# Performance work log

Measured on AMD Instinct MI355X. Metric: run time of the kernel, lower is better.

## Reference

```python
import jax, jax.numpy as jnp
import numpy as np

D_MODEL = 1024
D_STATE = 16
EXPAND = 2
D_INNER = D_MODEL * EXPAND
DT_RANK = D_MODEL // 16


def setup_inputs() -> dict:
    key = jax.random.key(0)
    ks = jax.random.split(key, 12)
    B, T = 2, 2048
    s_in = 1.0 / np.sqrt(D_MODEL)
    s_x = 1.0 / np.sqrt(D_INNER)
    s_dt = 1.0 / np.sqrt(DT_RANK)
    inp = {
        'u': jax.random.normal(ks[0], (B, T, D_MODEL), jnp.float32),
        'W_in': jax.random.uniform(ks[1], (2 * D_INNER, D_MODEL), jnp.float32, -s_in, s_in),
        'b_in': jax.random.uniform(ks[2], (2 * D_INNER,), jnp.float32, -s_in, s_in),
        'W_x': jax.random.uniform(ks[3], (DT_RANK + 2 * D_STATE, D_INNER), jnp.float32, -s_x, s_x),
        'b_x': jax.random.uniform(ks[4], (DT_RANK + 2 * D_STATE,), jnp.float32, -s_x, s_x),
        'W_dt': jax.random.uniform(ks[5], (D_INNER, DT_RANK), jnp.float32, -s_dt, s_dt),
        'b_dt': jax.random.uniform(ks[6], (D_INNER,), jnp.float32, -s_dt, s_dt),
        'A_log': jnp.log(jnp.abs(jax.random.normal(ks[7], (D_INNER, D_STATE), jnp.float32)) + 1e-6),
        'D': jnp.ones((D_INNER,), jnp.float32),
        'W_out': jax.random.uniform(ks[8], (D_MODEL, D_INNER), jnp.float32, -s_x, s_x),
        'b_out': jax.random.uniform(ks[9], (D_MODEL,), jnp.float32, -s_x, s_x),
    }
    return inp


def _ssm_forward(u, W_in, b_in, W_x, b_x, W_dt, b_dt, A_log, D, W_out, b_out):
    B, T, _ = u.shape
    u_inner = u @ W_in.T + b_in                       # [B,T,2*d_inner]
    x, z = jnp.split(u_inner, 2, axis=-1)             # each [B,T,d_inner]
    dbc = x @ W_x.T + b_x                             # [B,T,dt_rank+2N]
    delta_raw = dbc[..., :DT_RANK]
    B_ssm = dbc[..., DT_RANK:DT_RANK + D_STATE]       # [B,T,N]
    C_ssm = dbc[..., DT_RANK + D_STATE:]              # [B,T,N]
    delta = jax.nn.softplus(delta_raw @ W_dt.T + b_dt)  # [B,T,d_inner]
    A = -jnp.exp(A_log)                               # [d_inner,N]

    def step(h, xs):
        dt_t, x_t, Bt, Ct = xs                        # [B,d], [B,d], [B,N], [B,N]
        dA = jnp.exp(dt_t[..., None] * A)             # [B,d,N]
        dB = dt_t[..., None] * Bt[:, None, :]         # [B,d,N]
        h = h * dA + x_t[..., None] * dB
        y_t = jnp.einsum('bdn,bn->bd', h, Ct)
        return h, y_t

    h0 = jnp.zeros((B, D_INNER, D_STATE), u.dtype)
    xs = (jnp.swapaxes(delta, 0, 1), jnp.swapaxes(x, 0, 1),
          jnp.swapaxes(B_ssm, 0, 1), jnp.swapaxes(C_ssm, 0, 1))
    _, y = jax.lax.scan(step, h0, xs)                 # y: [T,B,d_inner]
    y = jnp.swapaxes(y, 0, 1)                         # [B,T,d_inner]
    y = y + x * D
    y = y * (z * jax.nn.sigmoid(z))                   # SiLU gate
    return y @ W_out.T + b_out                        # [B,T,d_model]


def reference(u, W_in, b_in, W_x, b_x, W_dt, b_dt, A_log, D, W_out, b_out):
    return _ssm_forward(u, W_in, b_in, W_x, b_x, W_dt, b_dt, A_log, D, W_out, b_out)
```

## Files before the change

kernel.cpp:

```cpp
#include <hip/hip_runtime.h>
#include <math.h>

#define BATCH 2
#define SEQ   2048
#define DM    1024
#define DI    2048
#define NST   16
#define MT    (BATCH*SEQ)
#define CHK   64
#define LCH   (SEQ/CHK)

typedef __attribute__((ext_vector_type(8))) short  bf16x8;
typedef __attribute__((ext_vector_type(4))) float  f32x4;

static __device__ __forceinline__ unsigned short f2bf(float f) {
  unsigned u = __float_as_uint(f);
  u += 0x7fff + ((u >> 16) & 1);
  return (unsigned short)(u >> 16);
}
static __device__ __forceinline__ float bf2f(unsigned short h) {
  return __uint_as_float(((unsigned)h) << 16);
}
static __device__ __forceinline__ float fexp2(float x) {
  float r;
  asm("v_exp_f32 %0, %1" : "=v"(r) : "v"(x));
  return r;
}
static __device__ __forceinline__ float flog2(float x) {
  float r;
  asm("v_log_f32 %0, %1" : "=v"(r) : "v"(x));
  return r;
}

#define SEG_U    (MT*DM/4)
#define SEG_WIN  (2*DI*DM/4)
#define SEG_WOUT (DM*DI/4)
#define SEG_WX   (96*DI/4)
#define SEG_WDT  (DI*64/4)
#define SEG_A    (DI*NST/4)
#define CUM0 SEG_U
#define CUM1 (CUM0+SEG_WIN)
#define CUM2 (CUM1+SEG_WOUT)
#define CUM3 (CUM2+SEG_WX)
#define CUM4 (CUM3+SEG_WDT)
#define CUM5 (CUM4+SEG_A)

__global__ __launch_bounds__(256) void convall_kernel(
    const float* __restrict__ u, const float* __restrict__ W_in,
    const float* __restrict__ W_out, const float* __restrict__ W_x,
    const float* __restrict__ W_dt, const float* __restrict__ A_log,
    unsigned short* __restrict__ u_bf, unsigned short* __restrict__ win_bf,
    unsigned short* __restrict__ wout_bf, unsigned short* __restrict__ wx_bf,
    unsigned short* __restrict__ wdt_bf, float* __restrict__ A2tab)
{
  const int gid = blockIdx.x*256 + threadIdx.x;
  const float4* src; ushort4* dst; int idx;
  if (gid < CUM0)      { idx = gid;        src = (const float4*)u;     dst = (ushort4*)u_bf; }
  else if (gid < CUM1) { idx = gid - CUM0; src = (const float4*)W_in;  dst = (ushort4*)win_bf; }
  else if (gid < CUM2) { idx = gid - CUM1; src = (const float4*)W_out; dst = (ushort4*)wout_bf; }
  else if (gid < CUM3) { idx = gid - CUM2; src = (const float4*)W_x;   dst = (ushort4*)wx_bf; }
  else if (gid < CUM4) { idx = gid - CUM3; src = (const float4*)W_dt;  dst = (ushort4*)wdt_bf; }
  else if (gid < CUM5) {
    int i = gid - CUM4;
    float4 v = ((const float4*)A_log)[i];
    float4 o;
    o.x = -1.44269504f * __expf(v.x);
    o.y = -1.44269504f * __expf(v.y);
    o.z = -1.44269504f * __expf(v.z);
    o.w = -1.44269504f * __expf(v.w);
    ((float4*)A2tab)[i] = o;
    return;
  } else return;
  float4 v = src[idx];
  ushort4 o;
  o.x = f2bf(v.x); o.y = f2bf(v.y); o.z = f2bf(v.z); o.w = f2bf(v.w);
  dst[idx] = o;
}

#define MEMFENCE asm volatile("" ::: "memory")

template<int K>
__global__ __launch_bounds__(512, 2) void gemm3_kernel(
    const unsigned short* __restrict__ A,
    const unsigned short* __restrict__ B,
    const float* __restrict__ bias,
    unsigned short* __restrict__ Cout, int nbx)
{
  extern __shared__ unsigned short smem[];
  unsigned short* As = smem;
  unsigned short* Bs = smem + 4*256*32;
  constexpr int NT = K / 32;

  const int nwg = gridDim.x;
  const int cpx = nwg >> 3;
  const int bid = blockIdx.x;
  const int swz = (bid & 7) * cpx + (bid >> 3);
  const int bx = swz % nbx;
  const int by = swz / nbx;

  const int tid  = threadIdx.x;
  const int lane = tid & 63;
  const int wid  = tid >> 6;
  const int wr   = wid >> 2;
  const int wc   = wid & 3;

  const size_t arow0 = (size_t)by * 256;
  const size_t brow0 = (size_t)bx * 256;

  const int s_r4 = lane >> 2;
  const int s_c  = lane & 3;

  auto STAGE_A = [&](int slot, int T) {
#pragma unroll
    for (int i = 0; i < 2; ++i) {
      const int r  = wid*32 + i*16 + s_r4;
      const int lc = s_c ^ ((r >> 1) & 3);
      const unsigned short* g = A + (arow0 + r)*(size_t)K + T*32 + lc*8;
      __builtin_amdgcn_global_load_lds(
          (const __attribute__((address_space(1))) void*)g,
          (__attribute__((address_space(3))) void*)(As + slot*(256*32) + (wid*32 + i*16)*32),
          16, 0, 0);
    }
  };
  auto STAGE_B = [&](int slot, int T) {
#pragma unroll
    for (int i = 0; i < 2; ++i) {
      const int r  = wid*32 + i*16 + s_r4;
      const int lc = s_c ^ ((r >> 1) & 3);
      const unsigned short* g = B + (brow0 + r)*(size_t)K + T*32 + lc*8;
      __builtin_amdgcn_global_load_lds(
          (const __attribute__((address_space(1))) void*)g,
          (__attribute__((address_space(3))) void*)(Bs + slot*(256*32) + (wid*32 + i*16)*32),
          16, 0, 0);
    }
  };

  f32x4 zero = {0.f, 0.f, 0.f, 0.f};
  f32x4 acc[8][4];
#pragma unroll
  for (int i = 0; i < 8; ++i)
#pragma unroll
    for (int j = 0; j < 4; ++j) acc[i][j] = zero;

  STAGE_A(0, 0); STAGE_B(0, 0);
  STAGE_A(1, 1); STAGE_B(1, 1);
  STAGE_A(2, 2); STAGE_B(2, 2);
  asm volatile("s_waitcnt vmcnt(8)" ::: "memory");
  __builtin_amdgcn_s_barrier();
  MEMFENCE;

  const int lrow = lane & 15, k8 = lane >> 4;
  bf16x8 bfr[4];

  for (int t = 0; t < NT; ++t) {
    const int slot = t & 3;
    const int sts  = (t + 3) & 3;
    const unsigned short* Asl = As + slot*(256*32);
    const unsigned short* Bsl = Bs + slot*(256*32);

    bf16x8 af[4];
#pragma unroll
    for (int nj = 0; nj < 4; ++nj) {
      const int r = wc*64 + nj*16 + lrow;
      bfr[nj] = *(const bf16x8*)&Bsl[r*32 + (k8 ^ ((r >> 1) & 3))*8];
    }
#pragma unroll
    for (int mi = 0; mi < 4; ++mi) {
      const int r = wr*128 + mi*16 + lrow;
      af[mi] = *(const bf16x8*)&Asl[r*32 + (k8 ^ ((r >> 1) & 3))*8];
    }
    if (t + 3 < NT) STAGE_A(sts, t + 3);
    MEMFENCE;
    __builtin_amdgcn_s_setprio(1);
#pragma unroll
    for (int mi = 0; mi < 4; ++mi)
#pragma unroll
      for (int nj = 0; nj < 4; ++nj)
        acc[mi][nj] = __builtin_amdgcn_mfma_f32_16x16x32_bf16(
                          af[mi], bfr[nj], acc[mi][nj], 0, 0, 0);
    __builtin_amdgcn_s_setprio(0);
    MEMFENCE;

#pragma unroll
    for (int mi = 0; mi < 4; ++mi) {
      const int r = wr*128 + 64 + mi*16 + lrow;
      af[mi] = *(const bf16x8*)&Asl[r*32 + (k8 ^ ((r >> 1) & 3))*8];
    }
    if (t + 3 < NT) STAGE_B(sts, t + 3);
    MEMFENCE;
    __builtin_amdgcn_s_setprio(1);
#pragma unroll
    for (int mi = 0; mi < 4; ++mi)
#pragma unroll
      for (int nj = 0; nj < 4; ++nj)
        acc[mi + 4][nj] = __builtin_amdgcn_mfma_f32_16x16x32_bf16(
                              af[mi], bfr[nj], acc[mi + 4][nj], 0, 0, 0);
    __builtin_amdgcn_s_setprio(0);

    if (t <= NT - 4)      asm volatile("s_waitcnt vmcnt(8)" ::: "memory");
    else if (t == NT - 3) asm volatile("s_waitcnt vmcnt(4)" ::: "memory");
    else                  asm volatile("s_waitcnt vmcnt(0)" ::: "memory");
    __builtin_amdgcn_s_barrier();
    MEMFENCE;
  }

  const int lcol = lane & 15, lrq = lane >> 4;
#pragma unroll
  for (int nj = 0; nj < 4; ++nj) {
    const int colg = bx*256 + wc*64 + nj*16 + lcol;
    const float bv = bias[colg];
#pragma unroll
    for (int mi = 0; mi < 8; ++mi) {
      const int rowg = by*256 + wr*128 + mi*16 + lrq*4;
#pragma unroll
      for (int q = 0; q < 4; ++q)
        Cout[(size_t)(rowg + q)*4096 + colg] = f2bf(acc[mi][nj][q] + bv);
    }
  }
}

template<int BN, int BK, bool OUT_BF16, int LDC, int ACT>
__global__ __launch_bounds__(256, 4) void gemm2_kernel(
    const unsigned short* __restrict__ A,
    const unsigned short* __restrict__ B,
    const float* __restrict__ bias,
    void* __restrict__ Cout, int K, int nbx)
{
  constexpr int NH = BK / 32;
  constexpr int NJ = BN / 32;
  __shared__ unsigned short Abuf[2][NH][128*32];
  __shared__ unsigned short Bbuf[2][NH][BN*32];

  const int nwg = gridDim.x;
  const int cpx = nwg >> 3;
  const int bid = blockIdx.x;
  const int swz = (bid & 7) * cpx + (bid >> 3);
  const int bx = swz % nbx;
  const int by = swz / nbx;

  const int tid  = threadIdx.x;
  const int lane = tid & 63;
  const int wid  = tid >> 6;
  const int wr   = wid >> 1;
  const int wc   = wid & 1;
  const int lr    = lane >> 2;
  const int lslot = lane & 3;

  f32x4 zero = {0.f, 0.f, 0.f, 0.f};
  f32x4 acc[4][NJ];
#pragma unroll
  for (int i = 0; i < 4; ++i)
#pragma unroll
    for (int j = 0; j < NJ; ++j) acc[i][j] = zero;

  const size_t arow0 = (size_t)by * 128;
  const size_t brow0 = (size_t)bx * BN;
  const int NT = K / BK;

  auto STAGE = [&](int buf, int k0) {
#pragma unroll
    for (int half = 0; half < NH; ++half) {
#pragma unroll
      for (int i = 0; i < 2; ++i) {
        const int Rb = (wid + i*4) * 16;
        const int r  = Rb + lr;
        const int c8 = lslot ^ ((r >> 1) & 3);
        const unsigned short* ga = A + (arow0 + r)*(size_t)K + k0 + half*32 + c8*8;
        __builtin_amdgcn_global_load_lds(
            (const __attribute__((address_space(1))) void*)ga,
            (__attribute__((address_space(3))) void*)(&Abuf[buf][half][Rb*32]),
            16, 0, 0);
      }
#pragma unroll
      for (int i = 0; i < BN/64; ++i) {
        const int Rb = (wid + i*4) * 16;
        const int r  = Rb + lr;
        const int c8 = lslot ^ ((r >> 1) & 3);
        const unsigned short* gb = B + (brow0 + r)*(size_t)K + k0 + half*32 + c8*8;
        __builtin_amdgcn_global_load_lds(
            (const __attribute__((address_space(1))) void*)gb,
            (__attribute__((address_space(3))) void*)(&Bbuf[buf][half][Rb*32]),
            16, 0, 0);
      }
    }
  };

  STAGE(0, 0);
  __syncthreads();

  const int lrow = lane & 15, k8 = lane >> 4;
  int cur = 0;
  for (int kt = 0; kt < NT; ++kt) {
    if (kt + 1 < NT) STAGE(cur ^ 1, (kt + 1) * BK);

#pragma unroll
    for (int half = 0; half < NH; ++half) {
      bf16x8 af[4], bfr[NJ];
#pragma unroll
      for (int mi = 0; mi < 4; ++mi) {
        const int r = wr*64 + mi*16 + lrow;
        af[mi] = *(const bf16x8*)&Abuf[cur][half][r*32 + (k8 ^ ((r >> 1) & 3))*8];
      }
#pragma unroll
      for (int nj = 0; nj < NJ; ++nj) {
        const int r = wc*(BN/2) + nj*16 + lrow;
        bfr[nj] = *(const bf16x8*)&Bbuf[cur][half][r*32 + (k8 ^ ((r >> 1) & 3))*8];
      }
      __builtin_amdgcn_s_setprio(1);
#pragma unroll
      for (int mi = 0; mi < 4; ++mi)
#pragma unroll
        for (int nj = 0; nj < NJ; ++nj)
          acc[mi][nj] = __builtin_amdgcn_mfma_f32_16x16x32_bf16(
                            af[mi], bfr[nj], acc[mi][nj], 0, 0, 0);
      __builtin_amdgcn_s_setprio(0);
    }
    __syncthreads();
    cur ^= 1;
  }

  const int lcol = lane & 15, lrq = lane >> 4;
#pragma unroll
  for (int nj = 0; nj < NJ; ++nj) {
    const int colg = bx*BN + wc*(BN/2) + nj*16 + lcol;
    const float bv = bias[colg];
#pragma unroll
    for (int mi = 0; mi < 4; ++mi) {
      const int rowg = by*128 + wr*64 + mi*16 + lrq*4;
#pragma unroll
      for (int q = 0; q < 4; ++q) {
        float v = acc[mi][nj][q] + bv;
        if constexpr (ACT == 1) {
          float e = fexp2(-1.44269504f * fabsf(v));
          v = fmaxf(v, 0.f) + 0.69314718f * flog2(1.f + e);
        }
        if constexpr (OUT_BF16)
          ((unsigned short*)Cout)[(size_t)(rowg + q)*LDC + colg] = f2bf(v);
        else
          ((float*)Cout)[(size_t)(rowg + q)*LDC + colg] = v;
      }
    }
  }
}

__global__ __launch_bounds__(256) void dbc_mfma_kernel(
    const unsigned short* __restrict__ A,
    const unsigned short* __restrict__ Bw,
    float* __restrict__ partial)
{
  __shared__ unsigned short Abuf[64*32];
  __shared__ unsigned short Bbuf[96*32];

  const int tid  = threadIdx.x;
  const int lane = tid & 63;
  const int wid  = tid >> 6;
  const int lr    = lane >> 2;
  const int lslot = lane & 3;
  const size_t arow0 = (size_t)blockIdx.x * 64;
  const int ks   = blockIdx.y;
  const int k0b  = ks * (DI/4);

  f32x4 zero = {0.f, 0.f, 0.f, 0.f};
  f32x4 acc[6];
#pragma unroll
  for (int j = 0; j < 6; ++j) acc[j] = zero;

  for (int k0 = k0b; k0 < k0b + DI/4; k0 += 32) {
    {
      const int Rb = wid*16;
      const int r  = Rb + lr;
      const int c8 = lslot ^ ((r >> 1) & 3);
      const unsigned short* ga = A + (arow0 + r)*4096 + k0 + c8*8;
      __builtin_amdgcn_global_load_lds(
          (const __attribute__((address_space(1))) void*)ga,
          (__attribute__((address_space(3))) void*)(Abuf + Rb*32), 16, 0, 0);
    }
    if (wid < 3) {
#pragma unroll
      for (int i = 0; i < 2; ++i) {
        const int Rb = wid*32 + i*16;
        const int r  = Rb + lr;
        const int c8 = lslot ^ ((r >> 1) & 3);
        const unsigned short* gb = Bw + (size_t)r*DI + k0 + c8*8;
        __builtin_amdgcn_global_load_lds(
            (const __attribute__((address_space(1))) void*)gb,
            (__attribute__((address_space(3))) void*)(Bbuf + Rb*32), 16, 0, 0);
      }
    }
    __syncthreads();

    const int lrow = lane & 15, k8 = lane >> 4;
    const int ra = wid*16 + lrow;
    bf16x8 af = *(const bf16x8*)&Abuf[ra*32 + (k8 ^ ((ra >> 1) & 3))*8];
#pragma unroll
    for (int nj = 0; nj < 6; ++nj) {
      const int rb = nj*16 + lrow;
      bf16x8 bf_ = *(const bf16x8*)&Bbuf[rb*32 + (k8 ^ ((rb >> 1) & 3))*8];
      acc[nj] = __builtin_amdgcn_mfma_f32_16x16x32_bf16(af, bf_, acc[nj], 0, 0, 0);
    }
    __syncthreads();
  }

  const int lcol = lane & 15, lrq = lane >> 4;
  const int rowg = (int)arow0 + wid*16 + lrq*4;
#pragma unroll
  for (int nj = 0; nj < 6; ++nj) {
    const int colg = nj*16 + lcol;
#pragma unroll
    for (int q = 0; q < 4; ++q)
      partial[((size_t)ks*MT + rowg + q)*96 + colg] = acc[nj][q];
  }
}

__global__ __launch_bounds__(256) void dbc_reduce_kernel(
    const float* __restrict__ partial, const float* __restrict__ bx,
    float* __restrict__ dbc, unsigned short* __restrict__ draw_bf)
{
  const int gid = blockIdx.x*256 + threadIdx.x;
  const int m = gid / 96;
  const int c = gid - m*96;
  const size_t stride = (size_t)MT*96;
  float s = partial[gid] + partial[gid + stride]
          + partial[gid + 2*stride] + partial[gid + 3*stride] + bx[c];
  if (c < 64) draw_bf[(size_t)m*64 + c] = f2bf(s);
  else        dbc[(size_t)m*96 + c] = s;
}

__global__ __launch_bounds__(256) void scanA_kernel(
    const unsigned short* __restrict__ uib,
    const float* __restrict__ dbc,
    const unsigned short* __restrict__ delta_bf,
    const float* __restrict__ A2tab,
    float* __restrict__ P,
    float* __restrict__ S)
{
  __shared__ float Bsh[LCH][16];
  const int bid = blockIdx.x;
  const int d   = (bid & 7)*256 + threadIdx.x;
  const int c   = (bid >> 3) & (CHK-1);
  const int b   = bid >> 9;
  const int t0  = c * LCH;

  {
    int i = threadIdx.x;
    if (i < LCH*4) {
      int st = i >> 2, p = i & 3;
      float4 v = *(const float4*)(dbc + ((size_t)b*SEQ + t0 + st)*96 + 64 + p*4);
      *(float4*)&Bsh[st][p*4] = v;
    }
  }

  float A2[NST];
  {
    const float4* ap = (const float4*)(A2tab + (size_t)d*NST);
#pragma unroll
    for (int q = 0; q < 4; ++q) {
      float4 v = ap[q];
      A2[q*4+0] = v.x; A2[q*4+1] = v.y; A2[q*4+2] = v.z; A2[q*4+3] = v.w;
    }
  }

  float h[NST];
#pragma unroll
  for (int nn = 0; nn < NST; ++nn) h[nn] = 0.f;
  float sdt = 0.f;

  const unsigned short* dptr = delta_bf + ((size_t)b*SEQ + t0)*DI + d;
  const unsigned short* xptr = uib      + ((size_t)b*SEQ + t0)*4096 + d;

  float dt = bf2f(dptr[0]);
  float xv = bf2f(xptr[0]);
  __syncthreads();

  for (int t = 0; t < LCH; ++t) {
    const float dtc = dt, xvc = xv;
    if (t + 1 < LCH) {
      const size_t tn = (size_t)(t+1);
      dt = bf2f(dptr[tn*DI]);
      xv = bf2f(xptr[tn*4096]);
    }
    float4 Bv0 = *(const float4*)&Bsh[t][0];
    float4 Bv1 = *(const float4*)&Bsh[t][4];
    float4 Bv2 = *(const float4*)&Bsh[t][8];
    float4 Bv3 = *(const float4*)&Bsh[t][12];
    float Bc[NST] = {Bv0.x,Bv0.y,Bv0.z,Bv0.w, Bv1.x,Bv1.y,Bv1.z,Bv1.w,
                     Bv2.x,Bv2.y,Bv2.z,Bv2.w, Bv3.x,Bv3.y,Bv3.z,Bv3.w};
    sdt += dtc;
    const float xdt = xvc * dtc;
#pragma unroll
    for (int nn = 0; nn < NST; ++nn) {
      float dA = fexp2(dtc * A2[nn]);
      h[nn] = h[nn]*dA + xdt*Bc[nn];
    }
  }

  float* Pp = P + (((size_t)b*CHK + c)*DI + d)*NST;
  float* Sp = S + (((size_t)b*CHK + c)*DI + d)*NST;
#pragma unroll
  for (int q = 0; q < 4; ++q) {
    float4 pv = { fexp2(A2[q*4+0]*sdt), fexp2(A2[q*4+1]*sdt),
                  fexp2(A2[q*4+2]*sdt), fexp2(A2[q*4+3]*sdt) };
    float4 sv = { h[q*4+0], h[q*4+1], h[q*4+2], h[q*4+3] };
    *(float4*)(Pp + q*4) = pv;
    *(float4*)(Sp + q*4) = sv;
  }
}

__global__ __launch_bounds__(256) void scanB_kernel(
    const float* __restrict__ P, float* __restrict__ S)
{
  const int gid = blockIdx.x*256 + threadIdx.x;
  const int n4 = gid & 3;
  const int d  = (gid >> 2) & (DI-1);
  const int b  = gid >> 13;

  float4 h = {0.f, 0.f, 0.f, 0.f};
  for (int c = 0; c < CHK; ++c) {
    const size_t idx = (((size_t)b*CHK + c)*DI + d)*NST + n4*4;
    float4 p = *(const float4*)(P + idx);
    float4 s = *(const float4*)(S + idx);
    *(float4*)(S + idx) = h;
    h.x = h.x*p.x + s.x;
    h.y = h.y*p.y + s.y;
    h.z = h.z*p.z + s.z;
    h.w = h.w*p.w + s.w;
  }
}

__global__ __launch_bounds__(256) void scanC_kernel(
    const unsigned short* __restrict__ uib,
    const float* __restrict__ dbc,
    const unsigned short* __restrict__ delta_bf,
    const float* __restrict__ A2tab,
    const float* __restrict__ Dp,
    const float* __restrict__ S,
    unsigned short* __restrict__ y_bf)
{
  __shared__ float BCs[LCH][32];
  const int bid = blockIdx.x;
  const int d   = (bid & 7)*256 + threadIdx.x;
  const int c   = (bid >> 3) & (CHK-1);
  const int b   = bid >> 9;
  const int t0  = c * LCH;

  {
    int i = threadIdx.x;
    int st = i >> 3, p = i & 7;
    float4 v = *(const float4*)(dbc + ((size_t)b*SEQ + t0 + st)*96 + 64 + p*4);
    *(float4*)&BCs[st][p*4] = v;
  }

  float A2[NST];
  {
    const float4* ap = (const float4*)(A2tab + (size_t)d*NST);
#pragma unroll
    for (int q = 0; q < 4; ++q) {
      float4 v = ap[q];
      A2[q*4+0] = v.x; A2[q*4+1] = v.y; A2[q*4+2] = v.z; A2[q*4+3] = v.w;
    }
  }
  const float Dv = Dp[d];

  float h[NST];
  {
    const float* Sp = S + (((size_t)b*CHK + c)*DI + d)*NST;
#pragma unroll
    for (int q = 0; q < 4; ++q) {
      float4 sv = *(const float4*)(Sp + q*4);
      h[q*4+0] = sv.x; h[q*4+1] = sv.y; h[q*4+2] = sv.z; h[q*4+3] = sv.w;
    }
  }

  const unsigned short* dptr = delta_bf + ((size_t)b*SEQ + t0)*DI + d;
  const unsigned short* xptr = uib      + ((size_t)b*SEQ + t0)*4096 + d;
  unsigned short* yp         = y_bf     + ((size_t)b*SEQ + t0)*DI + d;

  float dt = bf2f(dptr[0]);
  float xv = bf2f(xptr[0]);
  float zv = bf2f(xptr[2048]);
  __syncthreads();

  for (int t = 0; t < LCH; ++t) {
    const float dtc = dt, xvc = xv, zvc = zv;
    if (t + 1 < LCH) {
      const size_t tn = (size_t)(t+1);
      dt = bf2f(dptr[tn*DI]);
      xv = bf2f(xptr[tn*4096]);
      zv = bf2f(xptr[tn*4096 + 2048]);
    }
    float4 Bv0 = *(const float4*)&BCs[t][0];
    float4 Bv1 = *(const float4*)&BCs[t][4];
    float4 Bv2 = *(const float4*)&BCs[t][8];
    float4 Bv3 = *(const float4*)&BCs[t][12];
    float4 Cv0 = *(const float4*)&BCs[t][16];
    float4 Cv1 = *(const float4*)&BCs[t][20];
    float4 Cv2 = *(const float4*)&BCs[t][24];
    float4 Cv3 = *(const float4*)&BCs[t][28];
    float Bc[NST] = {Bv0.x,Bv0.y,Bv0.z,Bv0.w, Bv1.x,Bv1.y,Bv1.z,Bv1.w,
                     Bv2.x,Bv2.y,Bv2.z,Bv2.w, Bv3.x,Bv3.y,Bv3.z,Bv3.w};
    float Cc[NST] = {Cv0.x,Cv0.y,Cv0.z,Cv0.w, Cv1.x,Cv1.y,Cv1.z,Cv1.w,
                     Cv2.x,Cv2.y,Cv2.z,Cv2.w, Cv3.x,Cv3.y,Cv3.z,Cv3.w};
    const float xdt = xvc * dtc;
    float y = 0.f;
#pragma unroll
    for (int nn = 0; nn < NST; ++nn) {
      float dA = fexp2(dtc * A2[nn]);
      h[nn] = h[nn]*dA + xdt*Bc[nn];
      y += h[nn]*Cc[nn];
    }
    y += xvc * Dv;
    y *= zvc / (1.f + fexp2(-1.44269504f * zvc));
    yp[(size_t)t*DI] = f2bf(y);
  }
}

extern "C" void kernel_launch(void* const* d_in, const int* in_sizes, int n_in,
                              void* d_out, int out_size, void* d_ws, size_t ws_size,
                              hipStream_t stream)
{
  const float* u     = (const float*)d_in[0];
  const float* W_in  = (const float*)d_in[1];
  const float* b_in  = (const float*)d_in[2];
  const float* W_x   = (const float*)d_in[3];
  const float* b_x   = (const float*)d_in[4];
  const float* W_dt  = (const float*)d_in[5];
  const float* b_dt  = (const float*)d_in[6];
  const float* A_log = (const float*)d_in[7];
  const float* Dp    = (const float*)d_in[8];
  const float* W_out = (const float*)d_in[9];
  const float* b_out = (const float*)d_in[10];
  float* out = (float*)d_out;

  unsigned short* ui_bf    = (unsigned short*)d_ws;
  float*          dbc      = (float*)(ui_bf + (size_t)MT*4096);
  unsigned short* delta_bf = (unsigned short*)(dbc + (size_t)MT*96);
  unsigned short* y_bf     = delta_bf + (size_t)MT*DI;
  unsigned short* wout_bf  = y_bf + (size_t)MT*DI;
  unsigned short* wx_bf    = wout_bf + (size_t)DM*DI;
  unsigned short* wdt_bf   = wx_bf + (size_t)96*DI;
  unsigned short* draw_bf  = wdt_bf + (size_t)DI*64;
  float*          S        = (float*)(draw_bf + (size_t)MT*64);
  float*          A2tab    = S + (size_t)BATCH*CHK*DI*NST;
  float*          partial  = A2tab + (size_t)DI*NST;

  unsigned short* u_bf   = (unsigned short*)d_out;
  unsigned short* win_bf = u_bf + (size_t)MT*DM;
  float* P = (float*)d_out;

  convall_kernel<<<CUM5/256, 256, 0, stream>>>(
      u, W_in, W_out, W_x, W_dt, A_log,
      u_bf, win_bf, wout_bf, wx_bf, wdt_bf, A2tab);

  bool big = hipFuncSetAttribute(
      (const void*)gemm3_kernel<DM>,
      hipFuncAttributeMaxDynamicSharedMemorySize, 131072) == hipSuccess;
  if (big) {
    gemm3_kernel<DM><<<16*16, 512, 131072, stream>>>(
        u_bf, win_bf, b_in, ui_bf, 16);
  } else {
    gemm2_kernel<128, 32, true, 4096, 0><<<32*32, 256, 0, stream>>>(
        u_bf, win_bf, b_in, ui_bf, DM, 32);
  }

  dbc_mfma_kernel<<<dim3(MT/64, 4), 256, 0, stream>>>(ui_bf, wx_bf, partial);
  dbc_reduce_kernel<<<MT*96/256, 256, 0, stream>>>(partial, b_x, dbc, draw_bf);

  gemm2_kernel<128, 32, true, 2048, 1><<<16*32, 256, 0, stream>>>(
      draw_bf, wdt_bf, b_dt, delta_bf, 64, 16);

  scanA_kernel<<<BATCH*CHK*DI/256, 256, 0, stream>>>(ui_bf, dbc, delta_bf, A2tab, P, S);
  scanB_kernel<<<BATCH*DI*4/256, 256, 0, stream>>>(P, S);
  scanC_kernel<<<BATCH*CHK*DI/256, 256, 0, stream>>>(ui_bf, dbc, delta_bf, A2tab, Dp, S, y_bf);

  gemm2_kernel<64, 64, false, 1024, 0><<<16*32, 256, 0, stream>>>(
      y_bf, wout_bf, b_out, out, DI, 16);
}
```

Before: 183.3 us.

## Software-pipeline LDS fragment loads across k-tiles with ping-pong registers in gemm3

Restructures the gemm3 main loop to prefetch the next tile's B and first-half A fragments from LDS during the current tile, using double-buffered register sets and a two-step unrolled loop. It also adds barriers around each MFMA block, in a ping-pong style that interleaves wave groups, and changes the vmcnt wait threshold. The aim is to hide LDS read latency behind MFMA work. In exchange it raises register pressure and adds barriers, and the altered waitcnt and slot reuse may introduce hazards.

```diff
diff --git a/kernel.cpp b/kernel.cpp
--- a/kernel.cpp
+++ b/kernel.cpp
@@ -77,8 +77,6 @@
   dst[idx] = o;
 }
 
-#define MEMFENCE asm volatile("" ::: "memory")
-
 template<int K>
 __global__ __launch_bounds__(512, 2) void gemm3_kernel(
     const unsigned short* __restrict__ A,
@@ -147,62 +145,81 @@
   STAGE_A(2, 2); STAGE_B(2, 2);
   asm volatile("s_waitcnt vmcnt(8)" ::: "memory");
   __builtin_amdgcn_s_barrier();
-  MEMFENCE;
 
   const int lrow = lane & 15, k8 = lane >> 4;
-  bf16x8 bfr[4];
-
-  for (int t = 0; t < NT; ++t) {
-    const int slot = t & 3;
-    const int sts  = (t + 3) & 3;
-    const unsigned short* Asl = As + slot*(256*32);
-    const unsigned short* Bsl = Bs + slot*(256*32);
-
-    bf16x8 af[4];
-#pragma unroll
-    for (int nj = 0; nj < 4; ++nj) {
-      const int r = wc*64 + nj*16 + lrow;
-      bfr[nj] = *(const bf16x8*)&Bsl[r*32 + (k8 ^ ((r >> 1) & 3))*8];
-    }
-#pragma unroll
-    for (int mi = 0; mi < 4; ++mi) {
-      const int r = wr*128 + mi*16 + lrow;
-      af[mi] = *(const bf16x8*)&Asl[r*32 + (k8 ^ ((r >> 1) & 3))*8];
-    }
-    if (t + 3 < NT) STAGE_A(sts, t + 3);
-    MEMFENCE;
-    __builtin_amdgcn_s_setprio(1);
-#pragma unroll
-    for (int mi = 0; mi < 4; ++mi)
-#pragma unroll
-      for (int nj = 0; nj < 4; ++nj)
-        acc[mi][nj] = __builtin_amdgcn_mfma_f32_16x16x32_bf16(
-                          af[mi], bfr[nj], acc[mi][nj], 0, 0, 0);
-    __builtin_amdgcn_s_setprio(0);
-    MEMFENCE;
-
-#pragma unroll
-    for (int mi = 0; mi < 4; ++mi) {
-      const int r = wr*128 + 64 + mi*16 + lrow;
-      af[mi] = *(const bf16x8*)&Asl[r*32 + (k8 ^ ((r >> 1) & 3))*8];
-    }
-    if (t + 3 < NT) STAGE_B(sts, t + 3);
-    MEMFENCE;
-    __builtin_amdgcn_s_setprio(1);
-#pragma unroll
-    for (int mi = 0; mi < 4; ++mi)
-#pragma unroll
-      for (int nj = 0; nj < 4; ++nj)
-        acc[mi + 4][nj] = __builtin_amdgcn_mfma_f32_16x16x32_bf16(
-                              af[mi], bfr[nj], acc[mi + 4][nj], 0, 0, 0);
-    __builtin_amdgcn_s_setprio(0);
-
-    if (t <= NT - 4)      asm volatile("s_waitcnt vmcnt(8)" ::: "memory");
-    else if (t == NT - 3) asm volatile("s_waitcnt vmcnt(4)" ::: "memory");
-    else                  asm volatile("s_waitcnt vmcnt(0)" ::: "memory");
-    __builtin_amdgcn_s_barrier();
-    MEMFENCE;
-  }
+
+  bf16x8 af0A[4], af0B[4], bfrA[4], bfrB[4], af1[4];
+
+#pragma unroll
+  for (int nj = 0; nj < 4; ++nj) {
+    const int r = wc*64 + nj*16 + lrow;
+    bfrA[nj] = *(const bf16x8*)&Bs[r*32 + (k8 ^ ((r >> 1) & 3))*8];
+  }
+#pragma unroll
+  for (int mi = 0; mi < 4; ++mi) {
+    const int r = wr*128 + mi*16 + lrow;
+    af0A[mi] = *(const bf16x8*)&As[r*32 + (k8 ^ ((r >> 1) & 3))*8];
+  }
+
+#define TILE_BODY(T, AF0C, BFRC, AF0N, BFRN)                                   \
+  {                                                                            \
+    const int slot_ = (T) & 3;                                                 \
+    const unsigned short* Asl_ = As + slot_*(256*32);                          \
+         \
+    _Pragma("unroll")                                                          \
+    for (int mi = 0; mi < 4; ++mi) {                                           \
+      const int r = wr*128 + 64 + mi*16 + lrow;                                \
+      af1[mi] = *(const bf16x8*)&Asl_[r*32 + (k8 ^ ((r >> 1) & 3))*8];         \
+    }                                                                          \
+    if ((T) + 3 < NT) STAGE_A(((T)+3)&3, (T)+3);                               \
+    __builtin_amdgcn_s_barrier();                                              \
+    __builtin_amdgcn_s_setprio(1);                                             \
+    _Pragma("unroll")                                                          \
+    for (int mi = 0; mi < 4; ++mi)                                             \
+      _Pragma("unroll")                                                        \
+      for (int nj = 0; nj < 4; ++nj)                                           \
+        acc[mi][nj] = __builtin_amdgcn_mfma_f32_16x16x32_bf16(                 \
+                          AF0C[mi], BFRC[nj], acc[mi][nj], 0, 0, 0);           \
+    __builtin_amdgcn_s_setprio(0);                                             \
+    __builtin_amdgcn_s_barrier();                                              \
+      \
+     \
+    if ((T) + 1 < NT) {                                                        \
+      if ((T) <= NT - 4)      asm volatile("s_waitcnt vmcnt(6)" ::: "memory"); \
+      else if ((T) == NT - 3) asm volatile("s_waitcnt vmcnt(4)" ::: "memory"); \
+      else                    asm volatile("s_waitcnt vmcnt(0)" ::: "memory"); \
+      const int ns_ = ((T)+1) & 3;                                             \
+      const unsigned short* Asn_ = As + ns_*(256*32);                          \
+      const unsigned short* Bsn_ = Bs + ns_*(256*32);                          \
+      _Pragma("unroll")                                                        \
+      for (int nj = 0; nj < 4; ++nj) {                                         \
+        const int r = wc*64 + nj*16 + lrow;                                    \
+        BFRN[nj] = *(const bf16x8*)&Bsn_[r*32 + (k8 ^ ((r >> 1) & 3))*8];      \
+      }                                                                        \
+      _Pragma("unroll")                                                        \
+      for (int mi = 0; mi < 4; ++mi) {                                         \
+        const int r = wr*128 + mi*16 + lrow;                                   \
+        AF0N[mi] = *(const bf16x8*)&Asn_[r*32 + (k8 ^ ((r >> 1) & 3))*8];      \
+      }                                                                        \
+    }                                                                          \
+    if ((T) + 3 < NT) STAGE_B(((T)+3)&3, (T)+3);                               \
+    __builtin_amdgcn_s_barrier();                                              \
+    __builtin_amdgcn_s_setprio(1);                                             \
+    _Pragma("unroll")                                                          \
+    for (int mi = 0; mi < 4; ++mi)                                             \
+      _Pragma("unroll")                                                        \
+      for (int nj = 0; nj < 4; ++nj)                                           \
+        acc[mi+4][nj] = __builtin_amdgcn_mfma_f32_16x16x32_bf16(               \
+                          af1[mi], BFRC[nj], acc[mi+4][nj], 0, 0, 0);          \
+    __builtin_amdgcn_s_setprio(0);                                             \
+    __builtin_amdgcn_s_barrier();                                              \
+  }
+
+  for (int t = 0; t < NT; t += 2) {
+    TILE_BODY(t,     af0A, bfrA, af0B, bfrB);
+    TILE_BODY(t + 1, af0B, bfrB, af0A, bfrA);
+  }
+#undef TILE_BODY
 
   const int lcol = lane & 15, lrq = lane >> 4;
 #pragma unroll
```

Result: no change. 181.9 us (-0.7%).
